# Performance work log

Measured on AMD Instinct MI355X. Metric: run time of the kernel, lower is better.

The kernel has to match this reference:

```python
import jax, jax.numpy as jnp
import numpy as np

EPS = 0.0  # init eps


def setup_inputs() -> dict:
    key = jax.random.key(0)
    k1, k2 = jax.random.split(key)
    features = jax.random.normal(k1, (8, 64, 100000), dtype=jnp.float32)
    coords = jax.random.normal(k2, (8, 3, 100000), dtype=jnp.float32)
    return {"features": features, "coords": coords, "resolution": 32}


def _voxelize(features, coords, r):
    # coords: [B, 3, N], features: [B, C, N]
    coords = jax.lax.stop_gradient(coords)  # original does coords.detach()
    norm_coords = coords - jnp.mean(coords, axis=2, keepdims=True)
    # normalize=True branch: divide by 2*max point radius, shift to [0,1]
    radius = jnp.linalg.norm(norm_coords, axis=1, keepdims=True)        # [B,1,N]
    scale = jnp.max(radius, axis=2, keepdims=True) * 2.0 + EPS          # [B,1,1]
    norm_coords = norm_coords / scale + 0.5
    norm_coords = jnp.clip(norm_coords * r, 0, r - 1)                   # [B,3,N]
    vox = jnp.round(norm_coords).astype(jnp.int32)                      # [B,3,N]

    B, C, N = features.shape
    flat_idx = (vox[:, 0] * r + vox[:, 1]) * r + vox[:, 2]              # [B,N]
    seg_ids = (flat_idx + jnp.arange(B, dtype=jnp.int32)[:, None] * (r ** 3)).reshape(-1)

    feats = jnp.transpose(features, (0, 2, 1)).reshape(B * N, C)        # [B*N,C]
    sums = jax.ops.segment_sum(feats, seg_ids, num_segments=B * r ** 3)  # [B*r^3,C]
    cnts = jax.ops.segment_sum(jnp.ones((B * N,), features.dtype), seg_ids,
                               num_segments=B * r ** 3)                  # [B*r^3]
    avg = sums / jnp.maximum(cnts, 1.0)[:, None]
    vox_feat = jnp.transpose(avg.reshape(B, r ** 3, C), (0, 2, 1)).reshape(B, C, r, r, r)
    return vox_feat, norm_coords


def reference(features, coords, resolution):
    return _voxelize(features, coords, int(resolution))
```

## Files before the change

### kernel.cpp

```cpp
#include <hip/hip_runtime.h>
#include <math.h>

static constexpr int B = 8;
static constexpr int C = 64;
static constexpr int N = 100000;
static constexpr int RES = 32;
static constexpr int R3 = RES * RES * RES;
static constexpr int NQ = N / 4;

static constexpr int   SCALE_BITS = 19;
static constexpr float FSCALE     = (float)(1 << SCALE_BITS);
static constexpr float INV_FSCALE = 1.0f / FSCALE;

typedef float vfloat4 __attribute__((ext_vector_type(4)));

static constexpr size_t MEAN_OFF = 0;
static constexpr size_t MAX_OFF  = 192;
static constexpr size_t CNT_OFF  = 256;
static constexpr size_t VID_OFF  = CNT_OFF + (size_t)B * R3 * sizeof(int);
static constexpr size_t HDR_BYTES = 256;

__device__ __forceinline__ int vhash(int v) { return v ^ (v >> 5) ^ (v >> 10); }

__device__ __forceinline__ double block_reduce_sum(double v) {
    for (int off = 32; off > 0; off >>= 1) v += __shfl_down(v, off, 64);
    __shared__ double s[4];
    int lane = threadIdx.x & 63, w = threadIdx.x >> 6;
    if (lane == 0) s[w] = v;
    __syncthreads();
    if (threadIdx.x == 0) v = (s[0] + s[1]) + (s[2] + s[3]);
    return v;
}

__device__ __forceinline__ float block_reduce_max(float v) {
    for (int off = 32; off > 0; off >>= 1) v = fmaxf(v, __shfl_down(v, off, 64));
    __shared__ float s[4];
    int lane = threadIdx.x & 63, w = threadIdx.x >> 6;
    if (lane == 0) s[w] = v;
    __syncthreads();
    if (threadIdx.x == 0) v = fmaxf(fmaxf(s[0], s[1]), fmaxf(s[2], s[3]));
    return v;
}

__global__ void k_mean(const float* __restrict__ coords, double* __restrict__ mean_sum,
                       int* __restrict__ cnt) {
    int gtid = blockIdx.x * blockDim.x + threadIdx.x;
    int4* c4 = (int4*)cnt;
    for (int i = gtid; i < B * R3 / 4; i += gridDim.x * blockDim.x)
        c4[i] = make_int4(0, 0, 0, 0);

    const int NSLICE = 8;
    int pair  = blockIdx.x % (B * 3);
    int slice = blockIdx.x / (B * 3);
    const float* p = coords + (size_t)pair * N;
    double acc = 0.0;
#pragma unroll 4
    for (int i = slice * 256 + threadIdx.x; i < N; i += NSLICE * 256)
        acc += (double)p[i];
    acc = block_reduce_sum(acc);
    if (threadIdx.x == 0) atomicAdd(&mean_sum[pair], acc);
}

__global__ void k_max(const float* __restrict__ coords,
                      const double* __restrict__ mean_sum,
                      unsigned int* __restrict__ maxr2) {
    const int NSLICE = 16;
    int b     = blockIdx.x % B;
    int slice = blockIdx.x / B;
    __shared__ float sm[3];
    if (threadIdx.x < 3)
        sm[threadIdx.x] = (float)(mean_sum[b * 3 + threadIdx.x] / (double)N);
    __syncthreads();
    float mx = sm[0], my = sm[1], mz = sm[2];
    const float4* px = (const float4*)(coords + (size_t)(b * 3 + 0) * N);
    const float4* py = (const float4*)(coords + (size_t)(b * 3 + 1) * N);
    const float4* pz = (const float4*)(coords + (size_t)(b * 3 + 2) * N);
    float m = 0.0f;
    for (int i = slice * 256 + threadIdx.x; i < NQ; i += NSLICE * 256) {
        float4 x4 = px[i], y4 = py[i], z4 = pz[i];
        float x, y, z;
        x = x4.x - mx; y = y4.x - my; z = z4.x - mz; m = fmaxf(m, x*x + y*y + z*z);
        x = x4.y - mx; y = y4.y - my; z = z4.y - mz; m = fmaxf(m, x*x + y*y + z*z);
        x = x4.z - mx; y = y4.z - my; z = z4.z - mz; m = fmaxf(m, x*x + y*y + z*z);
        x = x4.w - mx; y = y4.w - my; z = z4.w - mz; m = fmaxf(m, x*x + y*y + z*z);
    }
    m = block_reduce_max(m);
    if (threadIdx.x == 0) atomicMax(&maxr2[b], __float_as_uint(m));
}

__global__ __launch_bounds__(256) void k_vid(const float* __restrict__ coords,
                      const double* __restrict__ mean_sum,
                      const unsigned int* __restrict__ maxr2,
                      unsigned short* __restrict__ vid,
                      float* __restrict__ out_norm,
                      int* __restrict__ cnt) {
    int b = blockIdx.y;
    __shared__ float sm[4];
    if (threadIdx.x < 3)
        sm[threadIdx.x] = (float)(mean_sum[b * 3 + threadIdx.x] / (double)N);
    if (threadIdx.x == 3)
        sm[3] = 2.0f * sqrtf(__uint_as_float(maxr2[b]));
    __syncthreads();
    int q = blockIdx.x * 256 + threadIdx.x;
    if (q >= NQ) return;
    float m0 = sm[0], m1 = sm[1], m2 = sm[2], scale = sm[3];

    const float4* p0 = (const float4*)(coords + (size_t)(b * 3 + 0) * N);
    const float4* p1 = (const float4*)(coords + (size_t)(b * 3 + 1) * N);
    const float4* p2 = (const float4*)(coords + (size_t)(b * 3 + 2) * N);
    float4* o0 = (float4*)(out_norm + (size_t)(b * 3 + 0) * N);
    float4* o1 = (float4*)(out_norm + (size_t)(b * 3 + 1) * N);
    float4* o2 = (float4*)(out_norm + (size_t)(b * 3 + 2) * N);
    float4 x4 = p0[q], y4 = p1[q], z4 = p2[q];

#define NORM1(v, mm) { v = (v - mm) / scale + 0.5f; v = v * (float)RES;     \
                       v = fminf(fmaxf(v, 0.0f), (float)(RES - 1)); }
    NORM1(x4.x, m0); NORM1(x4.y, m0); NORM1(x4.z, m0); NORM1(x4.w, m0);
    NORM1(y4.x, m1); NORM1(y4.y, m1); NORM1(y4.z, m1); NORM1(y4.w, m1);
    NORM1(z4.x, m2); NORM1(z4.y, m2); NORM1(z4.z, m2); NORM1(z4.w, m2);
#undef NORM1
    o0[q] = x4; o1[q] = y4; o2[q] = z4;

    int* cb = cnt + (size_t)b * R3;
    int f0 = ((int)rintf(x4.x) * RES + (int)rintf(y4.x)) * RES + (int)rintf(z4.x);
    int f1 = ((int)rintf(x4.y) * RES + (int)rintf(y4.y)) * RES + (int)rintf(z4.y);
    int f2 = ((int)rintf(x4.z) * RES + (int)rintf(y4.z)) * RES + (int)rintf(z4.z);
    int f3 = ((int)rintf(x4.w) * RES + (int)rintf(y4.w)) * RES + (int)rintf(z4.w);
    ushort4 h;
    h.x = (unsigned short)vhash(f0); h.y = (unsigned short)vhash(f1);
    h.z = (unsigned short)vhash(f2); h.w = (unsigned short)vhash(f3);
    ((ushort4*)(vid + (size_t)b * N))[q] = h;
    atomicAdd(&cb[f0], 1); atomicAdd(&cb[f1], 1);
    atomicAdd(&cb[f2], 1); atomicAdd(&cb[f3], 1);
}

__global__ __launch_bounds__(1024, 4) void k_accum(const unsigned short* __restrict__ vid,
                                                   const float* __restrict__ feats,
                                                   const int* __restrict__ cnt,
                                                   float* __restrict__ out_vox) {
    extern __shared__ char smem[];
    int* grid = (int*)smem;
    constexpr int BS = 1024, U = 6, STEP = BS * U;
    constexpr int NITER = 4;
    constexpr int NMAIN = NITER * STEP;
    int b = blockIdx.x & 7;
    int c = blockIdx.x >> 3;
    const uint2*   vp = (const uint2*)(vid + (size_t)b * N);
    const vfloat4* fp = (const vfloat4*)(feats + ((size_t)(b * C + c)) * N);
    const int tid = threadIdx.x;

    uint2 vA[U], vB[U]; vfloat4 fA[U], fB[U];

#define LOADC(dstv, dstf, chunk)                                            \
    {   int _base = (chunk) * STEP + tid;                                   \
        _Pragma("unroll")                                                   \
        for (int u = 0; u < U; ++u) {                                       \
            dstv[u] = vp[_base + u * BS];                                   \
            dstf[u] = __builtin_nontemporal_load(&fp[_base + u * BS]);      \
        } }
#define PROC(sv, sf)                                                        \
    {   _Pragma("unroll")                                                   \
        for (int u = 0; u < U; ++u) {                                       \
            uint2 vv = sv[u]; vfloat4 ff = sf[u];                           \
            atomicAdd(&grid[(int)(vv.x & 0xffffu)], __float2int_rn(ff.x * FSCALE)); \
            atomicAdd(&grid[(int)(vv.x >> 16)],     __float2int_rn(ff.y * FSCALE)); \
            atomicAdd(&grid[(int)(vv.y & 0xffffu)], __float2int_rn(ff.z * FSCALE)); \
            atomicAdd(&grid[(int)(vv.y >> 16)],     __float2int_rn(ff.w * FSCALE)); \
        } }

    LOADC(vA, fA, 0);
    LOADC(vB, fB, 1);
    int4* g4 = (int4*)grid;
    for (int i = tid; i < R3 / 4; i += BS) g4[i] = make_int4(0, 0, 0, 0);
    __syncthreads();

    __builtin_amdgcn_sched_barrier(0);
    PROC(vA, fA);
    LOADC(vA, fA, 2);
    __builtin_amdgcn_sched_barrier(0);
    PROC(vB, fB);
    LOADC(vB, fB, 3);
    __builtin_amdgcn_sched_barrier(0);
    PROC(vA, fA);
    __builtin_amdgcn_sched_barrier(0);
    PROC(vB, fB);
#undef LOADC
#undef PROC

    for (int i = NMAIN + tid; i < NQ; i += BS) {
        uint2 v = vp[i];
        vfloat4 f = __builtin_nontemporal_load(&fp[i]);
        atomicAdd(&grid[(int)(v.x & 0xffffu)], __float2int_rn(f.x * FSCALE));
        atomicAdd(&grid[(int)(v.x >> 16)],     __float2int_rn(f.y * FSCALE));
        atomicAdd(&grid[(int)(v.y & 0xffffu)], __float2int_rn(f.z * FSCALE));
        atomicAdd(&grid[(int)(v.y >> 16)],     __float2int_rn(f.w * FSCALE));
    }
    __syncthreads();

    const int4* cp4 = (const int4*)(cnt + (size_t)b * R3);
    float4* op4 = (float4*)(out_vox + ((size_t)(b * C + c)) * R3);
    for (int i = tid; i < R3 / 4; i += BS) {
        int4 c4v = cp4[i];
        int base = i * 4;
        float4 o;
        o.x = ((float)grid[vhash(base + 0)] * INV_FSCALE) / fmaxf((float)c4v.x, 1.0f);
        o.y = ((float)grid[vhash(base + 1)] * INV_FSCALE) / fmaxf((float)c4v.y, 1.0f);
        o.z = ((float)grid[vhash(base + 2)] * INV_FSCALE) / fmaxf((float)c4v.z, 1.0f);
        o.w = ((float)grid[vhash(base + 3)] * INV_FSCALE) / fmaxf((float)c4v.w, 1.0f);
        op4[i] = o;
    }
}

extern "C" void kernel_launch(void* const* d_in, const int* in_sizes, int n_in,
                              void* d_out, int out_size, void* d_ws, size_t ws_size,
                              hipStream_t stream) {
    const float* feats  = (const float*)d_in[0];
    const float* coords = (const float*)d_in[1];
    float* out_vox  = (float*)d_out;
    float* out_norm = out_vox + (size_t)B * C * R3;

    double*         mean_sum = (double*)((char*)d_ws + MEAN_OFF);
    unsigned int*   maxr2    = (unsigned int*)((char*)d_ws + MAX_OFF);
    int*            cnt      = (int*)((char*)d_ws + CNT_OFF);
    unsigned short* vid      = (unsigned short*)((char*)d_ws + VID_OFF);

    static bool attr_done = false;
    if (!attr_done) {
        (void)hipFuncSetAttribute((const void*)k_accum,
                            hipFuncAttributeMaxDynamicSharedMemorySize, R3 * sizeof(int));
        attr_done = true;
    }

    (void)hipMemsetAsync(d_ws, 0, HDR_BYTES, stream);

    k_mean<<<B * 3 * 8, 256, 0, stream>>>(coords, mean_sum, cnt);
    k_max<<<B * 16, 256, 0, stream>>>(coords, mean_sum, maxr2);
    k_vid<<<dim3((NQ + 255) / 256, B), 256, 0, stream>>>(coords, mean_sum, maxr2, vid, out_norm, cnt);
    k_accum<<<B * C, 1024, R3 * sizeof(int), stream>>>(vid, feats, cnt, out_vox);
}
```

Before: 357.0 us.

## Fuse mean, max-radius and voxel-id kernels into one persistent kernel with grid barriers

Merges the three front-end kernels (coordinate mean, max radius, normalize/voxel-id/count) into a single 120-block kernel that uses atomic spin grid barriers between phases, removing two kernel launches and their gaps. The final phase has each block loop over all 8 batches instead of using a 2D grid. The voxel output stores in the accumulation kernel also become nontemporal. The spin barrier only works if all 120 blocks are co-resident, and the front phases now have less parallelism per phase than the separate launches did.

```diff
diff --git a/kernel.cpp b/kernel.cpp
--- a/kernel.cpp
+++ b/kernel.cpp
@@ -16,9 +16,12 @@
 
 static constexpr size_t MEAN_OFF = 0;
 static constexpr size_t MAX_OFF  = 192;
+static constexpr size_t BAR_OFF  = 224;
 static constexpr size_t CNT_OFF  = 256;
 static constexpr size_t VID_OFF  = CNT_OFF + (size_t)B * R3 * sizeof(int);
 static constexpr size_t HDR_BYTES = 256;
+
+static constexpr int FRONT_BLOCKS = 120;
 
 __device__ __forceinline__ int vhash(int v) { return v ^ (v >> 5) ^ (v >> 10); }
 
@@ -42,96 +45,117 @@
     return v;
 }
 
-__global__ void k_mean(const float* __restrict__ coords, double* __restrict__ mean_sum,
-                       int* __restrict__ cnt) {
-    int gtid = blockIdx.x * blockDim.x + threadIdx.x;
-    int4* c4 = (int4*)cnt;
-    for (int i = gtid; i < B * R3 / 4; i += gridDim.x * blockDim.x)
-        c4[i] = make_int4(0, 0, 0, 0);
-
-    const int NSLICE = 8;
-    int pair  = blockIdx.x % (B * 3);
-    int slice = blockIdx.x / (B * 3);
-    const float* p = coords + (size_t)pair * N;
-    double acc = 0.0;
-#pragma unroll 4
-    for (int i = slice * 256 + threadIdx.x; i < N; i += NSLICE * 256)
-        acc += (double)p[i];
-    acc = block_reduce_sum(acc);
-    if (threadIdx.x == 0) atomicAdd(&mean_sum[pair], acc);
-}
-
-__global__ void k_max(const float* __restrict__ coords,
-                      const double* __restrict__ mean_sum,
-                      unsigned int* __restrict__ maxr2) {
-    const int NSLICE = 16;
-    int b     = blockIdx.x % B;
-    int slice = blockIdx.x / B;
-    __shared__ float sm[3];
-    if (threadIdx.x < 3)
-        sm[threadIdx.x] = (float)(mean_sum[b * 3 + threadIdx.x] / (double)N);
-    __syncthreads();
-    float mx = sm[0], my = sm[1], mz = sm[2];
-    const float4* px = (const float4*)(coords + (size_t)(b * 3 + 0) * N);
-    const float4* py = (const float4*)(coords + (size_t)(b * 3 + 1) * N);
-    const float4* pz = (const float4*)(coords + (size_t)(b * 3 + 2) * N);
-    float m = 0.0f;
-    for (int i = slice * 256 + threadIdx.x; i < NQ; i += NSLICE * 256) {
-        float4 x4 = px[i], y4 = py[i], z4 = pz[i];
-        float x, y, z;
-        x = x4.x - mx; y = y4.x - my; z = z4.x - mz; m = fmaxf(m, x*x + y*y + z*z);
-        x = x4.y - mx; y = y4.y - my; z = z4.y - mz; m = fmaxf(m, x*x + y*y + z*z);
-        x = x4.z - mx; y = y4.z - my; z = z4.z - mz; m = fmaxf(m, x*x + y*y + z*z);
-        x = x4.w - mx; y = y4.w - my; z = z4.w - mz; m = fmaxf(m, x*x + y*y + z*z);
-    }
-    m = block_reduce_max(m);
-    if (threadIdx.x == 0) atomicMax(&maxr2[b], __float_as_uint(m));
-}
-
-__global__ __launch_bounds__(256) void k_vid(const float* __restrict__ coords,
-                      const double* __restrict__ mean_sum,
-                      const unsigned int* __restrict__ maxr2,
-                      unsigned short* __restrict__ vid,
-                      float* __restrict__ out_norm,
-                      int* __restrict__ cnt) {
-    int b = blockIdx.y;
-    __shared__ float sm[4];
-    if (threadIdx.x < 3)
-        sm[threadIdx.x] = (float)(mean_sum[b * 3 + threadIdx.x] / (double)N);
-    if (threadIdx.x == 3)
-        sm[3] = 2.0f * sqrtf(__uint_as_float(maxr2[b]));
-    __syncthreads();
-    int q = blockIdx.x * 256 + threadIdx.x;
-    if (q >= NQ) return;
-    float m0 = sm[0], m1 = sm[1], m2 = sm[2], scale = sm[3];
-
-    const float4* p0 = (const float4*)(coords + (size_t)(b * 3 + 0) * N);
-    const float4* p1 = (const float4*)(coords + (size_t)(b * 3 + 1) * N);
-    const float4* p2 = (const float4*)(coords + (size_t)(b * 3 + 2) * N);
-    float4* o0 = (float4*)(out_norm + (size_t)(b * 3 + 0) * N);
-    float4* o1 = (float4*)(out_norm + (size_t)(b * 3 + 1) * N);
-    float4* o2 = (float4*)(out_norm + (size_t)(b * 3 + 2) * N);
-    float4 x4 = p0[q], y4 = p1[q], z4 = p2[q];
+__device__ __forceinline__ void grid_spin_barrier(unsigned int* bar, unsigned int target) {
+    __syncthreads();
+    if (threadIdx.x == 0) {
+        __threadfence();
+        atomicAdd(bar, 1u);
+        while (__hip_atomic_load(bar, __ATOMIC_ACQUIRE, __HIP_MEMORY_SCOPE_AGENT) < target)
+            __builtin_amdgcn_s_sleep(8);
+    }
+    __syncthreads();
+}
+
+__global__ __launch_bounds__(256) void k_front(const float* __restrict__ coords,
+                                               double* __restrict__ mean_sum,
+                                               unsigned int* __restrict__ maxr2,
+                                               unsigned short* __restrict__ vid,
+                                               float* __restrict__ out_norm,
+                                               int* __restrict__ cnt,
+                                               unsigned int* __restrict__ bar) {
+    const int bid = blockIdx.x, tid = threadIdx.x;
+
+    {
+        int gtid = bid * 256 + tid;
+        int4* c4 = (int4*)cnt;
+        for (int i = gtid; i < B * R3 / 4; i += FRONT_BLOCKS * 256)
+            c4[i] = make_int4(0, 0, 0, 0);
+
+        int pair  = bid % (B * 3);
+        int slice = bid / (B * 3);
+        const float4* p = (const float4*)(coords + (size_t)pair * N);
+        double acc = 0.0;
+        for (int i = slice * 256 + tid; i < NQ; i += 5 * 256) {
+            float4 v = p[i];
+            acc += (double)v.x; acc += (double)v.y;
+            acc += (double)v.z; acc += (double)v.w;
+        }
+        acc = block_reduce_sum(acc);
+        if (tid == 0) atomicAdd(&mean_sum[pair], acc);
+    }
+    grid_spin_barrier(bar, FRONT_BLOCKS);
+
+    {
+        int b     = bid % B;
+        int slice = bid / B;
+        __shared__ float sm[3];
+        if (tid < 3)
+            sm[tid] = (float)(__hip_atomic_load(&mean_sum[b * 3 + tid],
+                        __ATOMIC_RELAXED, __HIP_MEMORY_SCOPE_AGENT) / (double)N);
+        __syncthreads();
+        float mx = sm[0], my = sm[1], mz = sm[2];
+        const float4* px = (const float4*)(coords + (size_t)(b * 3 + 0) * N);
+        const float4* py = (const float4*)(coords + (size_t)(b * 3 + 1) * N);
+        const float4* pz = (const float4*)(coords + (size_t)(b * 3 + 2) * N);
+        float m = 0.0f;
+        for (int i = slice * 256 + tid; i < NQ; i += 15 * 256) {
+            float4 x4 = px[i], y4 = py[i], z4 = pz[i];
+            float x, y, z;
+            x = x4.x - mx; y = y4.x - my; z = z4.x - mz; m = fmaxf(m, x*x + y*y + z*z);
+            x = x4.y - mx; y = y4.y - my; z = z4.y - mz; m = fmaxf(m, x*x + y*y + z*z);
+            x = x4.z - mx; y = y4.z - my; z = z4.z - mz; m = fmaxf(m, x*x + y*y + z*z);
+            x = x4.w - mx; y = y4.w - my; z = z4.w - mz; m = fmaxf(m, x*x + y*y + z*z);
+        }
+        m = block_reduce_max(m);
+        if (tid == 0) atomicMax(&maxr2[b], __float_as_uint(m));
+    }
+    grid_spin_barrier(bar, 2 * FRONT_BLOCKS);
+
+    {
+        __shared__ float smm[8][3];
+        __shared__ float sms[8];
+        if (tid < 24)
+            smm[tid / 3][tid % 3] = (float)(__hip_atomic_load(&mean_sum[tid],
+                        __ATOMIC_RELAXED, __HIP_MEMORY_SCOPE_AGENT) / (double)N);
+        if (tid >= 32 && tid < 40)
+            sms[tid - 32] = 2.0f * sqrtf(__uint_as_float(__hip_atomic_load(
+                        &maxr2[tid - 32], __ATOMIC_RELAXED, __HIP_MEMORY_SCOPE_AGENT)));
+        __syncthreads();
+
+        int q = bid * 256 + tid;
+        if (q < NQ) {
+            for (int b = 0; b < B; ++b) {
+                float m0 = smm[b][0], m1 = smm[b][1], m2 = smm[b][2], scale = sms[b];
+                const float4* p0 = (const float4*)(coords + (size_t)(b * 3 + 0) * N);
+                const float4* p1 = (const float4*)(coords + (size_t)(b * 3 + 1) * N);
+                const float4* p2 = (const float4*)(coords + (size_t)(b * 3 + 2) * N);
+                float4* o0 = (float4*)(out_norm + (size_t)(b * 3 + 0) * N);
+                float4* o1 = (float4*)(out_norm + (size_t)(b * 3 + 1) * N);
+                float4* o2 = (float4*)(out_norm + (size_t)(b * 3 + 2) * N);
+                float4 x4 = p0[q], y4 = p1[q], z4 = p2[q];
 
 #define NORM1(v, mm) { v = (v - mm) / scale + 0.5f; v = v * (float)RES;     \
                        v = fminf(fmaxf(v, 0.0f), (float)(RES - 1)); }
-    NORM1(x4.x, m0); NORM1(x4.y, m0); NORM1(x4.z, m0); NORM1(x4.w, m0);
-    NORM1(y4.x, m1); NORM1(y4.y, m1); NORM1(y4.z, m1); NORM1(y4.w, m1);
-    NORM1(z4.x, m2); NORM1(z4.y, m2); NORM1(z4.z, m2); NORM1(z4.w, m2);
+                NORM1(x4.x, m0); NORM1(x4.y, m0); NORM1(x4.z, m0); NORM1(x4.w, m0);
+                NORM1(y4.x, m1); NORM1(y4.y, m1); NORM1(y4.z, m1); NORM1(y4.w, m1);
+                NORM1(z4.x, m2); NORM1(z4.y, m2); NORM1(z4.z, m2); NORM1(z4.w, m2);
 #undef NORM1
-    o0[q] = x4; o1[q] = y4; o2[q] = z4;
-
-    int* cb = cnt + (size_t)b * R3;
-    int f0 = ((int)rintf(x4.x) * RES + (int)rintf(y4.x)) * RES + (int)rintf(z4.x);
-    int f1 = ((int)rintf(x4.y) * RES + (int)rintf(y4.y)) * RES + (int)rintf(z4.y);
-    int f2 = ((int)rintf(x4.z) * RES + (int)rintf(y4.z)) * RES + (int)rintf(z4.z);
-    int f3 = ((int)rintf(x4.w) * RES + (int)rintf(y4.w)) * RES + (int)rintf(z4.w);
-    ushort4 h;
-    h.x = (unsigned short)vhash(f0); h.y = (unsigned short)vhash(f1);
-    h.z = (unsigned short)vhash(f2); h.w = (unsigned short)vhash(f3);
-    ((ushort4*)(vid + (size_t)b * N))[q] = h;
-    atomicAdd(&cb[f0], 1); atomicAdd(&cb[f1], 1);
-    atomicAdd(&cb[f2], 1); atomicAdd(&cb[f3], 1);
+                o0[q] = x4; o1[q] = y4; o2[q] = z4;
+
+                int* cb = cnt + (size_t)b * R3;
+                int f0 = ((int)rintf(x4.x) * RES + (int)rintf(y4.x)) * RES + (int)rintf(z4.x);
+                int f1 = ((int)rintf(x4.y) * RES + (int)rintf(y4.y)) * RES + (int)rintf(z4.y);
+                int f2 = ((int)rintf(x4.z) * RES + (int)rintf(y4.z)) * RES + (int)rintf(z4.z);
+                int f3 = ((int)rintf(x4.w) * RES + (int)rintf(y4.w)) * RES + (int)rintf(z4.w);
+                ushort4 h;
+                h.x = (unsigned short)vhash(f0); h.y = (unsigned short)vhash(f1);
+                h.z = (unsigned short)vhash(f2); h.w = (unsigned short)vhash(f3);
+                ((ushort4*)(vid + (size_t)b * N))[q] = h;
+                atomicAdd(&cb[f0], 1); atomicAdd(&cb[f1], 1);
+                atomicAdd(&cb[f2], 1); atomicAdd(&cb[f3], 1);
+            }
+        }
+    }
 }
 
 __global__ __launch_bounds__(1024, 4) void k_accum(const unsigned short* __restrict__ vid,
@@ -198,16 +222,16 @@
     __syncthreads();
 
     const int4* cp4 = (const int4*)(cnt + (size_t)b * R3);
-    float4* op4 = (float4*)(out_vox + ((size_t)(b * C + c)) * R3);
+    vfloat4* op4 = (vfloat4*)(out_vox + ((size_t)(b * C + c)) * R3);
     for (int i = tid; i < R3 / 4; i += BS) {
         int4 c4v = cp4[i];
         int base = i * 4;
-        float4 o;
+        vfloat4 o;
         o.x = ((float)grid[vhash(base + 0)] * INV_FSCALE) / fmaxf((float)c4v.x, 1.0f);
         o.y = ((float)grid[vhash(base + 1)] * INV_FSCALE) / fmaxf((float)c4v.y, 1.0f);
         o.z = ((float)grid[vhash(base + 2)] * INV_FSCALE) / fmaxf((float)c4v.z, 1.0f);
         o.w = ((float)grid[vhash(base + 3)] * INV_FSCALE) / fmaxf((float)c4v.w, 1.0f);
-        op4[i] = o;
+        __builtin_nontemporal_store(o, &op4[i]);
     }
 }
 
@@ -221,6 +245,7 @@
 
     double*         mean_sum = (double*)((char*)d_ws + MEAN_OFF);
     unsigned int*   maxr2    = (unsigned int*)((char*)d_ws + MAX_OFF);
+    unsigned int*   bar      = (unsigned int*)((char*)d_ws + BAR_OFF);
     int*            cnt      = (int*)((char*)d_ws + CNT_OFF);
     unsigned short* vid      = (unsigned short*)((char*)d_ws + VID_OFF);
 
@@ -233,8 +258,7 @@
 
     (void)hipMemsetAsync(d_ws, 0, HDR_BYTES, stream);
 
-    k_mean<<<B * 3 * 8, 256, 0, stream>>>(coords, mean_sum, cnt);
-    k_max<<<B * 16, 256, 0, stream>>>(coords, mean_sum, maxr2);
-    k_vid<<<dim3((NQ + 255) / 256, B), 256, 0, stream>>>(coords, mean_sum, maxr2, vid, out_norm, cnt);
+    k_front<<<FRONT_BLOCKS, 256, 0, stream>>>(coords, mean_sum, maxr2, vid,
+                                              out_norm, cnt, bar);
     k_accum<<<B * C, 1024, R3 * sizeof(int), stream>>>(vid, feats, cnt, out_vox);
 }
```

New measurement: 388.3 us. 1.09x slower.

## Process two channels per accum block and replace atomic reductions with partials

Applied to the files above, without the earlier changes.

k_accum now handles two channels per block (256 blocks instead of 512), prefetching the second channel's first chunks while it finishes the first channel's tail and writes its epilogue, so that global loads overlap the LDS readout. Output stores become nontemporal. The mean and max reductions write per-slice partials that consumers sum or max themselves, which removes the memset and the global atomics. The cost is half as many blocks, which may lower occupancy and load balance across CUs, and some redundant partial reduction in every consumer block.

```diff
diff --git a/kernel.cpp b/kernel.cpp
--- a/kernel.cpp
+++ b/kernel.cpp
@@ -14,11 +14,10 @@
 
 typedef float vfloat4 __attribute__((ext_vector_type(4)));
 
-static constexpr size_t MEAN_OFF = 0;
-static constexpr size_t MAX_OFF  = 192;
-static constexpr size_t CNT_OFF  = 256;
-static constexpr size_t VID_OFF  = CNT_OFF + (size_t)B * R3 * sizeof(int);
-static constexpr size_t HDR_BYTES = 256;
+static constexpr size_t MEANP_OFF = 0;
+static constexpr size_t MAXP_OFF  = 1536;
+static constexpr size_t CNT_OFF   = 2048;
+static constexpr size_t VID_OFF   = CNT_OFF + (size_t)B * R3 * sizeof(int);
 
 __device__ __forceinline__ int vhash(int v) { return v ^ (v >> 5) ^ (v >> 10); }
 
@@ -42,7 +41,7 @@
     return v;
 }
 
-__global__ void k_mean(const float* __restrict__ coords, double* __restrict__ mean_sum,
+__global__ void k_mean(const float* __restrict__ coords, double* __restrict__ mean_part,
                        int* __restrict__ cnt) {
     int gtid = blockIdx.x * blockDim.x + threadIdx.x;
     int4* c4 = (int4*)cnt;
@@ -58,18 +57,22 @@
     for (int i = slice * 256 + threadIdx.x; i < N; i += NSLICE * 256)
         acc += (double)p[i];
     acc = block_reduce_sum(acc);
-    if (threadIdx.x == 0) atomicAdd(&mean_sum[pair], acc);
+    if (threadIdx.x == 0) mean_part[pair * 8 + slice] = acc;
 }
 
 __global__ void k_max(const float* __restrict__ coords,
-                      const double* __restrict__ mean_sum,
-                      unsigned int* __restrict__ maxr2) {
+                      const double* __restrict__ mean_part,
+                      float* __restrict__ max_part) {
     const int NSLICE = 16;
     int b     = blockIdx.x % B;
     int slice = blockIdx.x / B;
     __shared__ float sm[3];
-    if (threadIdx.x < 3)
-        sm[threadIdx.x] = (float)(mean_sum[b * 3 + threadIdx.x] / (double)N);
+    if (threadIdx.x < 3) {
+        double s = 0.0;
+#pragma unroll
+        for (int k = 0; k < 8; ++k) s += mean_part[(b * 3 + threadIdx.x) * 8 + k];
+        sm[threadIdx.x] = (float)(s / (double)N);
+    }
     __syncthreads();
     float mx = sm[0], my = sm[1], mz = sm[2];
     const float4* px = (const float4*)(coords + (size_t)(b * 3 + 0) * N);
@@ -85,21 +88,29 @@
         x = x4.w - mx; y = y4.w - my; z = z4.w - mz; m = fmaxf(m, x*x + y*y + z*z);
     }
     m = block_reduce_max(m);
-    if (threadIdx.x == 0) atomicMax(&maxr2[b], __float_as_uint(m));
+    if (threadIdx.x == 0) max_part[b * 16 + slice] = m;
 }
 
 __global__ __launch_bounds__(256) void k_vid(const float* __restrict__ coords,
-                      const double* __restrict__ mean_sum,
-                      const unsigned int* __restrict__ maxr2,
+                      const double* __restrict__ mean_part,
+                      const float* __restrict__ max_part,
                       unsigned short* __restrict__ vid,
                       float* __restrict__ out_norm,
                       int* __restrict__ cnt) {
     int b = blockIdx.y;
     __shared__ float sm[4];
-    if (threadIdx.x < 3)
-        sm[threadIdx.x] = (float)(mean_sum[b * 3 + threadIdx.x] / (double)N);
-    if (threadIdx.x == 3)
-        sm[3] = 2.0f * sqrtf(__uint_as_float(maxr2[b]));
+    if (threadIdx.x < 3) {
+        double s = 0.0;
+#pragma unroll
+        for (int k = 0; k < 8; ++k) s += mean_part[(b * 3 + threadIdx.x) * 8 + k];
+        sm[threadIdx.x] = (float)(s / (double)N);
+    }
+    if (threadIdx.x == 3) {
+        float m = max_part[b * 16];
+#pragma unroll
+        for (int k = 1; k < 16; ++k) m = fmaxf(m, max_part[b * 16 + k]);
+        sm[3] = 2.0f * sqrtf(m);
+    }
     __syncthreads();
     int q = blockIdx.x * 256 + threadIdx.x;
     if (q >= NQ) return;
@@ -143,15 +154,17 @@
     constexpr int BS = 1024, U = 6, STEP = BS * U;
     constexpr int NITER = 4;
     constexpr int NMAIN = NITER * STEP;
-    int b = blockIdx.x & 7;
-    int c = blockIdx.x >> 3;
-    const uint2*   vp = (const uint2*)(vid + (size_t)b * N);
-    const vfloat4* fp = (const vfloat4*)(feats + ((size_t)(b * C + c)) * N);
+    int b     = blockIdx.x & 7;
+    int cpair = blockIdx.x >> 3;
+    const uint2*   vp  = (const uint2*)(vid + (size_t)b * N);
+    const vfloat4* fp0 = (const vfloat4*)(feats + ((size_t)(b * C + cpair)) * N);
+    const vfloat4* fp1 = (const vfloat4*)(feats + ((size_t)(b * C + cpair + 32)) * N);
     const int tid = threadIdx.x;
+    const int4* cp4 = (const int4*)(cnt + (size_t)b * R3);
 
     uint2 vA[U], vB[U]; vfloat4 fA[U], fB[U];
 
-#define LOADC(dstv, dstf, chunk)                                            \
+#define LOADC(fp, dstv, dstf, chunk)                                        \
     {   int _base = (chunk) * STEP + tid;                                   \
         _Pragma("unroll")                                                   \
         for (int u = 0; u < U; ++u) {                                       \
@@ -167,48 +180,74 @@
             atomicAdd(&grid[(int)(vv.y & 0xffffu)], __float2int_rn(ff.z * FSCALE)); \
             atomicAdd(&grid[(int)(vv.y >> 16)],     __float2int_rn(ff.w * FSCALE)); \
         } }
-
-    LOADC(vA, fA, 0);
-    LOADC(vB, fB, 1);
-    int4* g4 = (int4*)grid;
-    for (int i = tid; i < R3 / 4; i += BS) g4[i] = make_int4(0, 0, 0, 0);
-    __syncthreads();
-
-    __builtin_amdgcn_sched_barrier(0);
-    PROC(vA, fA);
-    LOADC(vA, fA, 2);
-    __builtin_amdgcn_sched_barrier(0);
-    PROC(vB, fB);
-    LOADC(vB, fB, 3);
-    __builtin_amdgcn_sched_barrier(0);
-    PROC(vA, fA);
-    __builtin_amdgcn_sched_barrier(0);
-    PROC(vB, fB);
+#define TAIL(fp)                                                            \
+    for (int i = NMAIN + tid; i < NQ; i += BS) {                            \
+        uint2 v = vp[i];                                                    \
+        vfloat4 f = __builtin_nontemporal_load(&fp[i]);                     \
+        atomicAdd(&grid[(int)(v.x & 0xffffu)], __float2int_rn(f.x * FSCALE)); \
+        atomicAdd(&grid[(int)(v.x >> 16)],     __float2int_rn(f.y * FSCALE)); \
+        atomicAdd(&grid[(int)(v.y & 0xffffu)], __float2int_rn(f.z * FSCALE)); \
+        atomicAdd(&grid[(int)(v.y >> 16)],     __float2int_rn(f.w * FSCALE)); \
+    }
+#define EPI(c)                                                              \
+    {   vfloat4* op4 = (vfloat4*)(out_vox + ((size_t)(b * C + (c))) * R3);  \
+        for (int i = tid; i < R3 / 4; i += BS) {                            \
+            int4 c4v = cp4[i];                                              \
+            int base = i * 4;                                               \
+            vfloat4 o;                                                      \
+            o.x = ((float)grid[vhash(base + 0)] * INV_FSCALE) / fmaxf((float)c4v.x, 1.0f); \
+            o.y = ((float)grid[vhash(base + 1)] * INV_FSCALE) / fmaxf((float)c4v.y, 1.0f); \
+            o.z = ((float)grid[vhash(base + 2)] * INV_FSCALE) / fmaxf((float)c4v.z, 1.0f); \
+            o.w = ((float)grid[vhash(base + 3)] * INV_FSCALE) / fmaxf((float)c4v.w, 1.0f); \
+            __builtin_nontemporal_store(o, &op4[i]);                        \
+        } }
+#define ZEROGRID                                                            \
+    {   int4* g4 = (int4*)grid;                                             \
+        for (int i = tid; i < R3 / 4; i += BS) g4[i] = make_int4(0, 0, 0, 0); }
+
+    LOADC(fp0, vA, fA, 0);
+    LOADC(fp0, vB, fB, 1);
+    ZEROGRID;
+    __syncthreads();
+
+    __builtin_amdgcn_sched_barrier(0);
+    PROC(vA, fA);
+    LOADC(fp0, vA, fA, 2);
+    __builtin_amdgcn_sched_barrier(0);
+    PROC(vB, fB);
+    LOADC(fp0, vB, fB, 3);
+    __builtin_amdgcn_sched_barrier(0);
+    PROC(vA, fA);
+    __builtin_amdgcn_sched_barrier(0);
+    PROC(vB, fB);
+    TAIL(fp0);
+    LOADC(fp1, vA, fA, 0);
+    LOADC(fp1, vB, fB, 1);
+    __syncthreads();
+    EPI(cpair);
+    __syncthreads();
+    ZEROGRID;
+    __syncthreads();
+
+    __builtin_amdgcn_sched_barrier(0);
+    PROC(vA, fA);
+    LOADC(fp1, vA, fA, 2);
+    __builtin_amdgcn_sched_barrier(0);
+    PROC(vB, fB);
+    LOADC(fp1, vB, fB, 3);
+    __builtin_amdgcn_sched_barrier(0);
+    PROC(vA, fA);
+    __builtin_amdgcn_sched_barrier(0);
+    PROC(vB, fB);
+    TAIL(fp1);
+    __syncthreads();
+    EPI(cpair + 32);
+
 #undef LOADC
 #undef PROC
-
-    for (int i = NMAIN + tid; i < NQ; i += BS) {
-        uint2 v = vp[i];
-        vfloat4 f = __builtin_nontemporal_load(&fp[i]);
-        atomicAdd(&grid[(int)(v.x & 0xffffu)], __float2int_rn(f.x * FSCALE));
-        atomicAdd(&grid[(int)(v.x >> 16)],     __float2int_rn(f.y * FSCALE));
-        atomicAdd(&grid[(int)(v.y & 0xffffu)], __float2int_rn(f.z * FSCALE));
-        atomicAdd(&grid[(int)(v.y >> 16)],     __float2int_rn(f.w * FSCALE));
-    }
-    __syncthreads();
-
-    const int4* cp4 = (const int4*)(cnt + (size_t)b * R3);
-    float4* op4 = (float4*)(out_vox + ((size_t)(b * C + c)) * R3);
-    for (int i = tid; i < R3 / 4; i += BS) {
-        int4 c4v = cp4[i];
-        int base = i * 4;
-        float4 o;
-        o.x = ((float)grid[vhash(base + 0)] * INV_FSCALE) / fmaxf((float)c4v.x, 1.0f);
-        o.y = ((float)grid[vhash(base + 1)] * INV_FSCALE) / fmaxf((float)c4v.y, 1.0f);
-        o.z = ((float)grid[vhash(base + 2)] * INV_FSCALE) / fmaxf((float)c4v.z, 1.0f);
-        o.w = ((float)grid[vhash(base + 3)] * INV_FSCALE) / fmaxf((float)c4v.w, 1.0f);
-        op4[i] = o;
-    }
+#undef TAIL
+#undef EPI
+#undef ZEROGRID
 }
 
 extern "C" void kernel_launch(void* const* d_in, const int* in_sizes, int n_in,
@@ -219,10 +258,10 @@
     float* out_vox  = (float*)d_out;
     float* out_norm = out_vox + (size_t)B * C * R3;
 
-    double*         mean_sum = (double*)((char*)d_ws + MEAN_OFF);
-    unsigned int*   maxr2    = (unsigned int*)((char*)d_ws + MAX_OFF);
-    int*            cnt      = (int*)((char*)d_ws + CNT_OFF);
-    unsigned short* vid      = (unsigned short*)((char*)d_ws + VID_OFF);
+    double*         mean_part = (double*)((char*)d_ws + MEANP_OFF);
+    float*          max_part  = (float*)((char*)d_ws + MAXP_OFF);
+    int*            cnt       = (int*)((char*)d_ws + CNT_OFF);
+    unsigned short* vid       = (unsigned short*)((char*)d_ws + VID_OFF);
 
     static bool attr_done = false;
     if (!attr_done) {
@@ -231,10 +270,9 @@
         attr_done = true;
     }
 
-    (void)hipMemsetAsync(d_ws, 0, HDR_BYTES, stream);
-
-    k_mean<<<B * 3 * 8, 256, 0, stream>>>(coords, mean_sum, cnt);
-    k_max<<<B * 16, 256, 0, stream>>>(coords, mean_sum, maxr2);
-    k_vid<<<dim3((NQ + 255) / 256, B), 256, 0, stream>>>(coords, mean_sum, maxr2, vid, out_norm, cnt);
-    k_accum<<<B * C, 1024, R3 * sizeof(int), stream>>>(vid, feats, cnt, out_vox);
-}
+    k_mean<<<B * 3 * 8, 256, 0, stream>>>(coords, mean_part, cnt);
+    k_max<<<B * 16, 256, 0, stream>>>(coords, mean_part, max_part);
+    k_vid<<<dim3((NQ + 255) / 256, B), 256, 0, stream>>>(coords, mean_part, max_part,
+                                                         vid, out_norm, cnt);
+    k_accum<<<B * C / 2, 1024, R3 * sizeof(int), stream>>>(vid, feats, cnt, out_vox);
+}
```

Measured after the change: 373.5 us. +4.6%, slower.

## Replace global atomics with partial buffers and shared-memory count histogram kernel

Applied to the files above, without the earlier changes.

Mean and max reductions now write per-block partials to workspace instead of using global atomics. This removes the header memset and the atomic initialisation ordering. Voxel counts move out of k_vid's global atomics into a new k_cnt kernel, which histograms in LDS per batch and writes the count grid once. That drops the need to zero-fill the count buffer in k_mean. Output stores in k_accum become nontemporal. The trade-off is an extra launch and only 8 blocks for counting, which may underuse the GPU.

```diff
diff --git a/kernel.cpp b/kernel.cpp
--- a/kernel.cpp
+++ b/kernel.cpp
@@ -14,11 +14,10 @@
 
 typedef float vfloat4 __attribute__((ext_vector_type(4)));
 
-static constexpr size_t MEAN_OFF = 0;
-static constexpr size_t MAX_OFF  = 192;
-static constexpr size_t CNT_OFF  = 256;
-static constexpr size_t VID_OFF  = CNT_OFF + (size_t)B * R3 * sizeof(int);
-static constexpr size_t HDR_BYTES = 256;
+static constexpr size_t MEANP_OFF = 0;
+static constexpr size_t MAXP_OFF  = 1536;
+static constexpr size_t CNT_OFF   = 2048;
+static constexpr size_t VID_OFF   = CNT_OFF + (size_t)B * R3 * sizeof(int);
 
 __device__ __forceinline__ int vhash(int v) { return v ^ (v >> 5) ^ (v >> 10); }
 
@@ -42,13 +41,7 @@
     return v;
 }
 
-__global__ void k_mean(const float* __restrict__ coords, double* __restrict__ mean_sum,
-                       int* __restrict__ cnt) {
-    int gtid = blockIdx.x * blockDim.x + threadIdx.x;
-    int4* c4 = (int4*)cnt;
-    for (int i = gtid; i < B * R3 / 4; i += gridDim.x * blockDim.x)
-        c4[i] = make_int4(0, 0, 0, 0);
-
+__global__ void k_mean(const float* __restrict__ coords, double* __restrict__ mean_part) {
     const int NSLICE = 8;
     int pair  = blockIdx.x % (B * 3);
     int slice = blockIdx.x / (B * 3);
@@ -58,18 +51,22 @@
     for (int i = slice * 256 + threadIdx.x; i < N; i += NSLICE * 256)
         acc += (double)p[i];
     acc = block_reduce_sum(acc);
-    if (threadIdx.x == 0) atomicAdd(&mean_sum[pair], acc);
+    if (threadIdx.x == 0) mean_part[pair * 8 + slice] = acc;
 }
 
 __global__ void k_max(const float* __restrict__ coords,
-                      const double* __restrict__ mean_sum,
-                      unsigned int* __restrict__ maxr2) {
+                      const double* __restrict__ mean_part,
+                      float* __restrict__ max_part) {
     const int NSLICE = 16;
     int b     = blockIdx.x % B;
     int slice = blockIdx.x / B;
     __shared__ float sm[3];
-    if (threadIdx.x < 3)
-        sm[threadIdx.x] = (float)(mean_sum[b * 3 + threadIdx.x] / (double)N);
+    if (threadIdx.x < 3) {
+        double s = 0.0;
+#pragma unroll
+        for (int k = 0; k < 8; ++k) s += mean_part[(b * 3 + threadIdx.x) * 8 + k];
+        sm[threadIdx.x] = (float)(s / (double)N);
+    }
     __syncthreads();
     float mx = sm[0], my = sm[1], mz = sm[2];
     const float4* px = (const float4*)(coords + (size_t)(b * 3 + 0) * N);
@@ -85,21 +82,28 @@
         x = x4.w - mx; y = y4.w - my; z = z4.w - mz; m = fmaxf(m, x*x + y*y + z*z);
     }
     m = block_reduce_max(m);
-    if (threadIdx.x == 0) atomicMax(&maxr2[b], __float_as_uint(m));
+    if (threadIdx.x == 0) max_part[b * 16 + slice] = m;
 }
 
 __global__ __launch_bounds__(256) void k_vid(const float* __restrict__ coords,
-                      const double* __restrict__ mean_sum,
-                      const unsigned int* __restrict__ maxr2,
+                      const double* __restrict__ mean_part,
+                      const float* __restrict__ max_part,
                       unsigned short* __restrict__ vid,
-                      float* __restrict__ out_norm,
-                      int* __restrict__ cnt) {
+                      float* __restrict__ out_norm) {
     int b = blockIdx.y;
     __shared__ float sm[4];
-    if (threadIdx.x < 3)
-        sm[threadIdx.x] = (float)(mean_sum[b * 3 + threadIdx.x] / (double)N);
-    if (threadIdx.x == 3)
-        sm[3] = 2.0f * sqrtf(__uint_as_float(maxr2[b]));
+    if (threadIdx.x < 3) {
+        double s = 0.0;
+#pragma unroll
+        for (int k = 0; k < 8; ++k) s += mean_part[(b * 3 + threadIdx.x) * 8 + k];
+        sm[threadIdx.x] = (float)(s / (double)N);
+    }
+    if (threadIdx.x == 3) {
+        float m = max_part[b * 16];
+#pragma unroll
+        for (int k = 1; k < 16; ++k) m = fmaxf(m, max_part[b * 16 + k]);
+        sm[3] = 2.0f * sqrtf(m);
+    }
     __syncthreads();
     int q = blockIdx.x * 256 + threadIdx.x;
     if (q >= NQ) return;
@@ -121,7 +125,6 @@
 #undef NORM1
     o0[q] = x4; o1[q] = y4; o2[q] = z4;
 
-    int* cb = cnt + (size_t)b * R3;
     int f0 = ((int)rintf(x4.x) * RES + (int)rintf(y4.x)) * RES + (int)rintf(z4.x);
     int f1 = ((int)rintf(x4.y) * RES + (int)rintf(y4.y)) * RES + (int)rintf(z4.y);
     int f2 = ((int)rintf(x4.z) * RES + (int)rintf(y4.z)) * RES + (int)rintf(z4.z);
@@ -130,8 +133,27 @@
     h.x = (unsigned short)vhash(f0); h.y = (unsigned short)vhash(f1);
     h.z = (unsigned short)vhash(f2); h.w = (unsigned short)vhash(f3);
     ((ushort4*)(vid + (size_t)b * N))[q] = h;
-    atomicAdd(&cb[f0], 1); atomicAdd(&cb[f1], 1);
-    atomicAdd(&cb[f2], 1); atomicAdd(&cb[f3], 1);
+}
+
+__global__ __launch_bounds__(1024) void k_cnt(const unsigned short* __restrict__ vid,
+                                              int* __restrict__ cnt) {
+    extern __shared__ char smem[];
+    int* grid = (int*)smem;
+    const int b = blockIdx.x, tid = threadIdx.x;
+    int4* g4 = (int4*)grid;
+    for (int i = tid; i < R3 / 4; i += 1024) g4[i] = make_int4(0, 0, 0, 0);
+    __syncthreads();
+    const uint2* vp = (const uint2*)(vid + (size_t)b * N);
+    for (int i = tid; i < NQ; i += 1024) {
+        uint2 v = vp[i];
+        atomicAdd(&grid[(int)(v.x & 0xffffu)], 1);
+        atomicAdd(&grid[(int)(v.x >> 16)],     1);
+        atomicAdd(&grid[(int)(v.y & 0xffffu)], 1);
+        atomicAdd(&grid[(int)(v.y >> 16)],     1);
+    }
+    __syncthreads();
+    int* cb = cnt + (size_t)b * R3;
+    for (int i = tid; i < R3; i += 1024) cb[i] = grid[vhash(i)];
 }
 
 __global__ __launch_bounds__(1024, 4) void k_accum(const unsigned short* __restrict__ vid,
@@ -198,16 +220,16 @@
     __syncthreads();
 
     const int4* cp4 = (const int4*)(cnt + (size_t)b * R3);
-    float4* op4 = (float4*)(out_vox + ((size_t)(b * C + c)) * R3);
+    vfloat4* op4 = (vfloat4*)(out_vox + ((size_t)(b * C + c)) * R3);
     for (int i = tid; i < R3 / 4; i += BS) {
         int4 c4v = cp4[i];
         int base = i * 4;
-        float4 o;
+        vfloat4 o;
         o.x = ((float)grid[vhash(base + 0)] * INV_FSCALE) / fmaxf((float)c4v.x, 1.0f);
         o.y = ((float)grid[vhash(base + 1)] * INV_FSCALE) / fmaxf((float)c4v.y, 1.0f);
         o.z = ((float)grid[vhash(base + 2)] * INV_FSCALE) / fmaxf((float)c4v.z, 1.0f);
         o.w = ((float)grid[vhash(base + 3)] * INV_FSCALE) / fmaxf((float)c4v.w, 1.0f);
-        op4[i] = o;
+        __builtin_nontemporal_store(o, &op4[i]);
     }
 }
 
@@ -219,22 +241,24 @@
     float* out_vox  = (float*)d_out;
     float* out_norm = out_vox + (size_t)B * C * R3;
 
-    double*         mean_sum = (double*)((char*)d_ws + MEAN_OFF);
-    unsigned int*   maxr2    = (unsigned int*)((char*)d_ws + MAX_OFF);
-    int*            cnt      = (int*)((char*)d_ws + CNT_OFF);
-    unsigned short* vid      = (unsigned short*)((char*)d_ws + VID_OFF);
+    double*         mean_part = (double*)((char*)d_ws + MEANP_OFF);
+    float*          max_part  = (float*)((char*)d_ws + MAXP_OFF);
+    int*            cnt       = (int*)((char*)d_ws + CNT_OFF);
+    unsigned short* vid       = (unsigned short*)((char*)d_ws + VID_OFF);
 
     static bool attr_done = false;
     if (!attr_done) {
         (void)hipFuncSetAttribute((const void*)k_accum,
                             hipFuncAttributeMaxDynamicSharedMemorySize, R3 * sizeof(int));
+        (void)hipFuncSetAttribute((const void*)k_cnt,
+                            hipFuncAttributeMaxDynamicSharedMemorySize, R3 * sizeof(int));
         attr_done = true;
     }
 
-    (void)hipMemsetAsync(d_ws, 0, HDR_BYTES, stream);
-
-    k_mean<<<B * 3 * 8, 256, 0, stream>>>(coords, mean_sum, cnt);
-    k_max<<<B * 16, 256, 0, stream>>>(coords, mean_sum, maxr2);
-    k_vid<<<dim3((NQ + 255) / 256, B), 256, 0, stream>>>(coords, mean_sum, maxr2, vid, out_norm, cnt);
+    k_mean<<<B * 3 * 8, 256, 0, stream>>>(coords, mean_part);
+    k_max<<<B * 16, 256, 0, stream>>>(coords, mean_part, max_part);
+    k_vid<<<dim3((NQ + 255) / 256, B), 256, 0, stream>>>(coords, mean_part, max_part,
+                                                         vid, out_norm);
+    k_cnt<<<B, 1024, R3 * sizeof(int), stream>>>(vid, cnt);
     k_accum<<<B * C, 1024, R3 * sizeof(int), stream>>>(vid, feats, cnt, out_vox);
 }
```

After: 324.4 us. -9.1%, faster.
